# Kernel tuning notes

Measured on AMD Instinct MI355X. Metric: run time of the kernel, lower is better.

## Reference

```python
import jax, jax.numpy as jnp
import numpy as np

MAX_RANGE = 100.0


def _conv3x3(x, w, b):
    # x: [B,C,H,W], w: [2,C,3,3], b: [2]
    y = jax.lax.conv_general_dilated(
        x, w, window_strides=(1, 1), padding='SAME',
        dimension_numbers=('NCHW', 'OIHW', 'NCHW'))
    return y + b[None, :, None, None]


def setup_inputs() -> dict:
    key = jax.random.key(0)
    k1, k2, k3 = jax.random.split(key, 3)
    B, C, H, W = 4, 64, 64, 64
    x = jax.random.normal(k1, (B, C, H, W), dtype=jnp.float32)
    conv_w = jax.random.normal(k2, (2, C, 3, 3), dtype=jnp.float32) * 0.05
    conv_b = jax.random.normal(k3, (2,), dtype=jnp.float32) * 0.05
    return {'x': x, 'conv_w': conv_w, 'conv_b': conv_b}


def reference(x, conv_w, conv_b):
    # alpha, beta: [B,1,H,W]
    ab = MAX_RANGE * jnp.tanh(_conv3x3(x, conv_w, conv_b))
    alpha, beta = ab[:, 0:1], ab[:, 1:2]

    # Pairwise differences d[b,i,j,h,w] = beta[b]*x[b,i] - x[b,j]  -> [B,C,C,H,W]
    d = beta[:, :, None] * x[:, :, None] - x[:, None, :]
    a = alpha[:, :, None]  # [B,1,1,H,W]

    # softAbs: softmax over the pair {d, -d} weighted by clamped alpha*d logits
    v1 = jnp.clip(d * a, -MAX_RANGE, MAX_RANGE)
    v2 = jnp.clip(-d * a, -MAX_RANGE, MAX_RANGE)
    m = jnp.maximum(v1, v2)
    e1 = jnp.exp(v1 - m)
    e2 = jnp.exp(v2 - m)
    p1 = e1 / (e1 + e2)
    sabs = d * (2.0 * p1 - 1.0)  # d*p1 + (-d)*(1-p1)

    # mean over i (the expand dim) -> [B,C,H,W]
    tmp = jnp.mean(sabs, axis=1)

    # softArgMin over channel dim
    sam = jax.nn.softmax(jnp.clip(-tmp * alpha, -MAX_RANGE, MAX_RANGE), axis=1)

    # soft median, keepdims -> [B,1,H,W]
    return jnp.sum(x * sam, axis=1, keepdims=True)
```

## Files before the change

kernel.cpp:

```cpp
#include <hip/hip_runtime.h>
#include <math.h>

#define MAXR 100.0f
#define LOG2E 1.4426950408889634f

__device__ __forceinline__ float bcast_lane(float v, int i) {
    return __int_as_float(__builtin_amdgcn_readlane(__float_as_int(v), i));
}
__device__ __forceinline__ float exp2_fast(float x) { return __builtin_amdgcn_exp2f(x); }
__device__ __forceinline__ float rcp_fast(float x)  { return __builtin_amdgcn_rcpf(x); }

__device__ __forceinline__ float tanh_fast(float s) {
    float E = exp2_fast(2.0f * LOG2E * fabsf(s));
    float t = fmaf(-2.0f, rcp_fast(E + 1.0f), 1.0f);
    return copysignf(t, s);
}

__global__ __launch_bounds__(256) void dsf_fused(const float* __restrict__ x,
                                                 const float* __restrict__ wg,
                                                 const float* __restrict__ bias,
                                                 float* __restrict__ out) {
    __shared__ float xs[64 * 19];

    const int tid  = threadIdx.x;
    const int lane = tid & 63;
    const int wave = tid >> 6;

    const int p0 = blockIdx.x * 4;
    const int b  = p0 >> 12;
    const int h  = (p0 >> 6) & 63;
    const int w0 = p0 & 63;

    float wr0[9], wr1[9];
    #pragma unroll
    for (int k = 0; k < 9; ++k) {
        wr0[k] = wg[lane * 9 + k];
        wr1[k] = wg[576 + lane * 9 + k];
    }
    const float b0 = bias[0], b1 = bias[1];

    const float* xbase = x + b * 262144;
    for (int e = tid; e < 1152; e += 256) {
        int c   = e / 18;
        int rem = e - c * 18;
        int r   = rem / 6;
        int wt  = rem - r * 6;
        int hh  = h + r - 1;
        int ww  = w0 - 1 + wt;
        float v = 0.f;
        if (hh >= 0 && hh < 64 && ww >= 0 && ww < 64)
            v = xbase[c * 4096 + hh * 64 + ww];
        xs[c * 19 + rem] = v;
    }
    __syncthreads();

    const float* xc = xs + lane * 19;
    float a0 = 0.f, a1 = 0.f;
    #pragma unroll
    for (int r = 0; r < 3; ++r) {
        #pragma unroll
        for (int t = 0; t < 3; ++t) {
            float xv = xc[r * 6 + wave + t];
            a0 = fmaf(xv, wr0[r * 3 + t], a0);
            a1 = fmaf(xv, wr1[r * 3 + t], a1);
        }
    }
    #pragma unroll
    for (int off = 32; off; off >>= 1) {
        a0 += __shfl_xor(a0, off, 64);
        a1 += __shfl_xor(a1, off, 64);
    }
    const float al = MAXR * tanh_fast(a0 + b0);
    const float be = MAXR * tanh_fast(a1 + b1);
    const float aa = fabsf(al);
    const float c2 = 2.0f * LOG2E * aa;

    const float xj = xc[6 + wave + 1];

    float A0 = 0.f, A1 = 0.f, A2 = 0.f, A3 = 0.f;
    #pragma unroll
    for (int i = 0; i < 16; ++i) {
        float s0 = bcast_lane(xj, i);
        float s1 = bcast_lane(xj, i + 16);
        float s2 = bcast_lane(xj, i + 32);
        float s3 = bcast_lane(xj, i + 48);
        float d0 = fmaf(be, s0, -xj);
        float d1 = fmaf(be, s1, -xj);
        float d2 = fmaf(be, s2, -xj);
        float d3 = fmaf(be, s3, -xj);
        float E0 = exp2_fast(c2 * fabsf(d0));
        float E1 = exp2_fast(c2 * fabsf(d1));
        float E2 = exp2_fast(c2 * fabsf(d2));
        float E3 = exp2_fast(c2 * fabsf(d3));
        float r0 = rcp_fast(E0 + 1.f);
        float r1 = rcp_fast(E1 + 1.f);
        float r2 = rcp_fast(E2 + 1.f);
        float r3 = rcp_fast(E3 + 1.f);
        float u0 = fmaf(-2.f, r0, 1.f);
        float u1 = fmaf(-2.f, r1, 1.f);
        float u2 = fmaf(-2.f, r2, 1.f);
        float u3 = fmaf(-2.f, r3, 1.f);
        A0 = fmaf(fabsf(d0), u0, A0);
        A1 = fmaf(fabsf(d1), u1, A1);
        A2 = fmaf(fabsf(d2), u2, A2);
        A3 = fmaf(fabsf(d3), u3, A3);
    }
    float A = (A0 + A1) + (A2 + A3);

    float gl = fmaxf(-A * aa * (1.0f / 64.0f), -MAXR);

    float gm = gl;
    #pragma unroll
    for (int off = 32; off; off >>= 1) gm = fmaxf(gm, __shfl_xor(gm, off, 64));
    float ew  = exp2_fast((gl - gm) * LOG2E);
    float den = ew, num = xj * ew;
    #pragma unroll
    for (int off = 32; off; off >>= 1) {
        den += __shfl_xor(den, off, 64);
        num += __shfl_xor(num, off, 64);
    }
    if (lane == 0) out[p0 + wave] = num * rcp_fast(den);
}

extern "C" void kernel_launch(void* const* d_in, const int* in_sizes, int n_in,
                              void* d_out, int out_size, void* d_ws, size_t ws_size,
                              hipStream_t stream) {
    const float* x      = (const float*)d_in[0];
    const float* conv_w = (const float*)d_in[1];
    const float* conv_b = (const float*)d_in[2];
    float* out = (float*)d_out;
    (void)d_ws; (void)ws_size;

    dsf_fused<<<4096, 256, 0, stream>>>(x, conv_w, conv_b, out);
}
```

Measured before the change: 85.29 us.

## Process four pixels per wave and use DPP wave reductions

Each block now covers 16 consecutive pixels instead of 4, so each wave handles 4 pixels and the shared-memory halo tile is amortized across more outputs. Grid size drops by 4x. The block loads a wider window into registers and reuses the loaded conv weights across pixels. Shuffle-based reductions are replaced with DPP row-shift/broadcast sequences plus a readlane, and launch bounds now request occupancy. The risks are higher register pressure, more serialized per-wave work, and fewer blocks to fill the GPU.

```diff
diff --git a/kernel.cpp b/kernel.cpp
--- a/kernel.cpp
+++ b/kernel.cpp
@@ -4,11 +4,11 @@
 #define MAXR 100.0f
 #define LOG2E 1.4426950408889634f
 
+__device__ __forceinline__ float exp2_fast(float x) { return __builtin_amdgcn_exp2f(x); }
+__device__ __forceinline__ float rcp_fast(float x)  { return __builtin_amdgcn_rcpf(x); }
 __device__ __forceinline__ float bcast_lane(float v, int i) {
     return __int_as_float(__builtin_amdgcn_readlane(__float_as_int(v), i));
 }
-__device__ __forceinline__ float exp2_fast(float x) { return __builtin_amdgcn_exp2f(x); }
-__device__ __forceinline__ float rcp_fast(float x)  { return __builtin_amdgcn_rcpf(x); }
 
 __device__ __forceinline__ float tanh_fast(float s) {
     float E = exp2_fast(2.0f * LOG2E * fabsf(s));
@@ -16,17 +16,44 @@
     return copysignf(t, s);
 }
 
-__global__ __launch_bounds__(256) void dsf_fused(const float* __restrict__ x,
-                                                 const float* __restrict__ wg,
-                                                 const float* __restrict__ bias,
-                                                 float* __restrict__ out) {
-    __shared__ float xs[64 * 19];
+template<int CTRL>
+__device__ __forceinline__ float dpp0(float v) {
+    return __int_as_float(__builtin_amdgcn_update_dpp(0, __float_as_int(v), CTRL, 0xf, 0xf, true));
+}
+template<int CTRL>
+__device__ __forceinline__ float dppk(float v) {
+    return __int_as_float(__builtin_amdgcn_update_dpp(__float_as_int(v), __float_as_int(v), CTRL, 0xf, 0xf, false));
+}
+__device__ __forceinline__ float wave_sum(float v) {
+    v += dpp0<0x111>(v);
+    v += dpp0<0x112>(v);
+    v += dpp0<0x114>(v);
+    v += dpp0<0x118>(v);
+    v += dpp0<0x142>(v);
+    v += dpp0<0x143>(v);
+    return bcast_lane(v, 63);
+}
+__device__ __forceinline__ float wave_max(float v) {
+    v = fmaxf(v, dppk<0x111>(v));
+    v = fmaxf(v, dppk<0x112>(v));
+    v = fmaxf(v, dppk<0x114>(v));
+    v = fmaxf(v, dppk<0x118>(v));
+    v = fmaxf(v, dppk<0x142>(v));
+    v = fmaxf(v, dppk<0x143>(v));
+    return bcast_lane(v, 63);
+}
+
+__global__ __launch_bounds__(256, 4) void dsf_fused(const float* __restrict__ x,
+                                                    const float* __restrict__ wg,
+                                                    const float* __restrict__ bias,
+                                                    float* __restrict__ out) {
+    __shared__ float xs[64 * 57];
 
     const int tid  = threadIdx.x;
     const int lane = tid & 63;
     const int wave = tid >> 6;
 
-    const int p0 = blockIdx.x * 4;
+    const int p0 = blockIdx.x * 16;
     const int b  = p0 >> 12;
     const int h  = (p0 >> 6) & 63;
     const int w0 = p0 & 63;
@@ -40,86 +67,73 @@
     const float b0 = bias[0], b1 = bias[1];
 
     const float* xbase = x + b * 262144;
-    for (int e = tid; e < 1152; e += 256) {
-        int c   = e / 18;
-        int rem = e - c * 18;
-        int r   = rem / 6;
-        int wt  = rem - r * 6;
+    for (int e = tid; e < 3456; e += 256) {
+        int c   = e / 54;
+        int rem = e - c * 54;
+        int r   = rem / 18;
+        int wt  = rem - r * 18;
         int hh  = h + r - 1;
         int ww  = w0 - 1 + wt;
         float v = 0.f;
-        if (hh >= 0 && hh < 64 && ww >= 0 && ww < 64)
+        if (hh >= 0 && hh < 64 && (unsigned)ww < 64u)
             v = xbase[c * 4096 + hh * 64 + ww];
-        xs[c * 19 + rem] = v;
+        xs[c * 57 + r * 19 + wt] = v;
     }
     __syncthreads();
 
-    const float* xc = xs + lane * 19;
-    float a0 = 0.f, a1 = 0.f;
+    const float* xc = xs + lane * 57;
+    float win[3][6];
     #pragma unroll
-    for (int r = 0; r < 3; ++r) {
+    for (int r = 0; r < 3; ++r)
         #pragma unroll
-        for (int t = 0; t < 3; ++t) {
-            float xv = xc[r * 6 + wave + t];
-            a0 = fmaf(xv, wr0[r * 3 + t], a0);
-            a1 = fmaf(xv, wr1[r * 3 + t], a1);
+        for (int t = 0; t < 6; ++t)
+            win[r][t] = xc[r * 19 + wave * 4 + t];
+
+    float be[4], aa[4], c2[4], xj[4];
+    #pragma unroll
+    for (int p = 0; p < 4; ++p) {
+        float a0 = 0.f, a1 = 0.f;
+        #pragma unroll
+        for (int r = 0; r < 3; ++r) {
+            #pragma unroll
+            for (int t = 0; t < 3; ++t) {
+                float xv = win[r][p + t];
+                a0 = fmaf(xv, wr0[r * 3 + t], a0);
+                a1 = fmaf(xv, wr1[r * 3 + t], a1);
+            }
+        }
+        a0 = wave_sum(a0);
+        a1 = wave_sum(a1);
+        float al = MAXR * tanh_fast(a0 + b0);
+        be[p]    = MAXR * tanh_fast(a1 + b1);
+        aa[p]    = fabsf(al);
+        c2[p]    = 2.0f * LOG2E * aa[p];
+        xj[p]    = win[1][p + 1];
+    }
+
+    float A[4] = {0.f, 0.f, 0.f, 0.f};
+    #pragma unroll 4
+    for (int i = 0; i < 64; ++i) {
+        #pragma unroll
+        for (int p = 0; p < 4; ++p) {
+            float s = bcast_lane(xj[p], i);
+            float d = fmaf(be[p], s, -xj[p]);
+            float E = exp2_fast(c2[p] * fabsf(d));
+            float r = rcp_fast(E + 1.0f);
+            float u = fmaf(-2.0f, r, 1.0f);
+            A[p] = fmaf(fabsf(d), u, A[p]);
         }
     }
+
     #pragma unroll
-    for (int off = 32; off; off >>= 1) {
-        a0 += __shfl_xor(a0, off, 64);
-        a1 += __shfl_xor(a1, off, 64);
+    for (int p = 0; p < 4; ++p) {
+        float gl = fmaxf(-A[p] * aa[p] * (1.0f / 64.0f), -MAXR);
+        float gm = wave_max(gl);
+        float ew = exp2_fast((gl - gm) * LOG2E);
+        float den = wave_sum(ew);
+        float num = wave_sum(xj[p] * ew);
+        if (lane == 0) out[p0 + wave * 4 + p] = num * rcp_fast(den);
     }
-    const float al = MAXR * tanh_fast(a0 + b0);
-    const float be = MAXR * tanh_fast(a1 + b1);
-    const float aa = fabsf(al);
-    const float c2 = 2.0f * LOG2E * aa;
-
-    const float xj = xc[6 + wave + 1];
-
-    float A0 = 0.f, A1 = 0.f, A2 = 0.f, A3 = 0.f;
-    #pragma unroll
-    for (int i = 0; i < 16; ++i) {
-        float s0 = bcast_lane(xj, i);
-        float s1 = bcast_lane(xj, i + 16);
-        float s2 = bcast_lane(xj, i + 32);
-        float s3 = bcast_lane(xj, i + 48);
-        float d0 = fmaf(be, s0, -xj);
-        float d1 = fmaf(be, s1, -xj);
-        float d2 = fmaf(be, s2, -xj);
-        float d3 = fmaf(be, s3, -xj);
-        float E0 = exp2_fast(c2 * fabsf(d0));
-        float E1 = exp2_fast(c2 * fabsf(d1));
-        float E2 = exp2_fast(c2 * fabsf(d2));
-        float E3 = exp2_fast(c2 * fabsf(d3));
-        float r0 = rcp_fast(E0 + 1.f);
-        float r1 = rcp_fast(E1 + 1.f);
-        float r2 = rcp_fast(E2 + 1.f);
-        float r3 = rcp_fast(E3 + 1.f);
-        float u0 = fmaf(-2.f, r0, 1.f);
-        float u1 = fmaf(-2.f, r1, 1.f);
-        float u2 = fmaf(-2.f, r2, 1.f);
-        float u3 = fmaf(-2.f, r3, 1.f);
-        A0 = fmaf(fabsf(d0), u0, A0);
-        A1 = fmaf(fabsf(d1), u1, A1);
-        A2 = fmaf(fabsf(d2), u2, A2);
-        A3 = fmaf(fabsf(d3), u3, A3);
-    }
-    float A = (A0 + A1) + (A2 + A3);
-
-    float gl = fmaxf(-A * aa * (1.0f / 64.0f), -MAXR);
-
-    float gm = gl;
-    #pragma unroll
-    for (int off = 32; off; off >>= 1) gm = fmaxf(gm, __shfl_xor(gm, off, 64));
-    float ew  = exp2_fast((gl - gm) * LOG2E);
-    float den = ew, num = xj * ew;
-    #pragma unroll
-    for (int off = 32; off; off >>= 1) {
-        den += __shfl_xor(den, off, 64);
-        num += __shfl_xor(num, off, 64);
-    }
-    if (lane == 0) out[p0 + wave] = num * rcp_fast(den);
 }
 
 extern "C" void kernel_launch(void* const* d_in, const int* in_sizes, int n_in,
@@ -131,5 +145,5 @@
     float* out = (float*)d_out;
     (void)d_ws; (void)ws_size;
 
-    dsf_fused<<<4096, 256, 0, stream>>>(x, conv_w, conv_b, out);
+    dsf_fused<<<1024, 256, 0, stream>>>(x, conv_w, conv_b, out);
 }
```

Measured after the change: 86.24 us. No clear change (+1.1%).
